# Optimization experiments

Hardware: AMD Instinct MI355X
Metric: run time of the kernel (lower is better)

The kernel has to match this reference:

```python
import jax, jax.numpy as jnp
import numpy as np

N = 50000      # nodes
E = 800000     # directed edges (avg degree 16)
F_IN = 128     # dataset.num_features
H = 256        # hidden_channels
C = 40         # dataset.num_classes


def _glorot(k, shape):
    lim = float(np.sqrt(6.0 / (shape[0] + shape[1])))
    return jax.random.uniform(k, shape, jnp.float32, -lim, lim)


def setup_inputs() -> dict:
    key = jax.random.key(0)
    ks = jax.random.split(key, 8)
    x = jax.random.normal(ks[0], (N, F_IN), jnp.float32)
    edge_index = jax.random.randint(ks[1], (2, E), 0, N, dtype=jnp.int32)
    W1 = _glorot(ks[2], (F_IN, H));      b1 = jnp.zeros((H,), jnp.float32)
    W2 = _glorot(ks[3], (H, H // 2));    b2 = jnp.zeros((H // 2,), jnp.float32)
    W3 = _glorot(ks[4], (H // 2, H // 4)); b3 = jnp.zeros((H // 4,), jnp.float32)
    W4 = _glorot(ks[5], (H // 4, C));    b4 = jnp.zeros((C,), jnp.float32)
    return {"x": x, "edge_index": edge_index,
            "W1": W1, "b1": b1, "W2": W2, "b2": b2,
            "W3": W3, "b3": b3, "W4": W4, "b4": b4}


def reference(x, edge_index, W1, b1, W2, b2, W3, b3, W4, b4):
    # GCNConv with default add_self_loops=True and symmetric normalization.
    loops = jnp.arange(N, dtype=edge_index.dtype)
    src = jnp.concatenate([edge_index[0], loops])   # message sources
    dst = jnp.concatenate([edge_index[1], loops])   # aggregation targets
    # degree computed on target index (PyG default), incl. self-loops
    deg = jax.ops.segment_sum(jnp.ones_like(dst, jnp.float32), dst, num_segments=N)
    dinv = jnp.where(deg > 0, jax.lax.rsqrt(deg), 0.0)
    norm = dinv[src] * dinv[dst]                    # [E+N]

    def conv(h, W, b):
        h = h @ W                                   # transform first (PyG order)
        msg = h[src] * norm[:, None]                # gather + scale
        return jax.ops.segment_sum(msg, dst, num_segments=N) + b

    h = jax.nn.relu(conv(x, W1, b1))   # dropout = identity in eval mode
    h = jax.nn.relu(conv(h, W2, b2))
    h = jax.nn.relu(conv(h, W3, b3))
    return conv(h, W4, b4)
```

## Files before the change

### kernel.cpp

```cpp
#include <hip/hip_runtime.h>
#include <stdint.h>

#define NNODES 50000
#define NEDGES 800000
#define NB ((NNODES + 255) / 256)
#define EPB 4096
#define SCAT_NBLK ((NEDGES + EPB - 1) / EPB)

typedef __attribute__((ext_vector_type(8))) short bf16x8;
typedef __attribute__((ext_vector_type(4))) float f32x4;

__device__ inline unsigned short f2bf(float f) {
    unsigned u = __float_as_uint(f);
    return (unsigned short)((u + 0x7fffu + ((u >> 16) & 1u)) >> 16);
}
__device__ inline float bf2f(unsigned short h) {
    return __uint_as_float(((unsigned)h) << 16);
}


__global__ void zero_kernel(int* __restrict__ p, int n) {
    int i = blockIdx.x * blockDim.x + threadIdx.x;
    if (i < n) p[i] = 0;
}

__global__ __launch_bounds__(256) void bucket_count_kernel(const int* __restrict__ dst,
                                                           int* __restrict__ bhist) {
    __shared__ int h[NB];
    for (int b = threadIdx.x; b < NB; b += 256) h[b] = 0;
    __syncthreads();
    const int base = blockIdx.x * EPB;
#pragma unroll
    for (int i = 0; i < EPB / 256; ++i) {
        const int e = base + threadIdx.x + i * 256;
        if (e < NEDGES) atomicAdd(&h[dst[e] >> 8], 1);
    }
    __syncthreads();
    for (int b = threadIdx.x; b < NB; b += 256)
        if (h[b]) atomicAdd(&bhist[b], h[b]);
}

__global__ __launch_bounds__(256) void bucket_scan_kernel(const int* __restrict__ bhist,
                                                          int* __restrict__ bofs,
                                                          int* __restrict__ gcur,
                                                          int* __restrict__ rp_last) {
    __shared__ int s[256];
    const int t = threadIdx.x;
    s[t] = (t < NB) ? bhist[t] : 0;
    __syncthreads();
    for (int off = 1; off < 256; off <<= 1) {
        int v = (t >= off) ? s[t - off] : 0;
        __syncthreads();
        s[t] += v;
        __syncthreads();
    }
    if (t < NB) {
        const int excl = (t > 0) ? s[t - 1] : 0;
        bofs[t] = excl;
        gcur[t] = excl;
    }
    if (t == 255) { bofs[NB] = s[255]; rp_last[0] = s[255]; }
}

__global__ __launch_bounds__(256) void bucket_scatter_kernel(const int* __restrict__ src,
                                                             const int* __restrict__ dst,
                                                             int* __restrict__ gcur,
                                                             unsigned* __restrict__ gpk) {
    __shared__ int h[256];
    __shared__ int s[256];
    __shared__ int gof[256];
    __shared__ unsigned pr[EPB];
    __shared__ int ga[EPB];

    const int t = threadIdx.x;
    const int base = blockIdx.x * EPB;
    const int nval = min(EPB, NEDGES - base);

    h[t] = 0;
    __syncthreads();
#pragma unroll
    for (int i = 0; i < EPB / 256; ++i) {
        const int e = base + t + i * 256;
        if (e < NEDGES) atomicAdd(&h[dst[e] >> 8], 1);
    }
    __syncthreads();
    s[t] = h[t];
    __syncthreads();
    for (int off = 1; off < 256; off <<= 1) {
        int v = (t >= off) ? s[t - off] : 0;
        __syncthreads();
        s[t] += v;
        __syncthreads();
    }
    {
        const int c = h[t];
        if (t < NB && c > 0) gof[t] = atomicAdd(&gcur[t], c);
        const int lofs = s[t] - c;
        h[t] = lofs;
        s[t] = lofs;
    }
    __syncthreads();
#pragma unroll
    for (int i = 0; i < EPB / 256; ++i) {
        const int e = base + t + i * 256;
        if (e < NEDGES) {
            const int d = dst[e];
            const int b = d >> 8;
            const int slot = atomicAdd(&h[b], 1);
            pr[slot] = ((unsigned)(d & 255) << 16) | (unsigned)src[e];
            ga[slot] = gof[b] + (slot - s[b]);
        }
    }
    __syncthreads();
#pragma unroll
    for (int i = 0; i < EPB / 256; ++i) {
        const int slot = t + i * 256;
        if (slot < nval) gpk[ga[slot]] = pr[slot];
    }
}

__global__ __launch_bounds__(256) void csr_fill_kernel(const unsigned* __restrict__ gpk,
                                                       const int* __restrict__ bofs,
                                                       int* __restrict__ rp,
                                                       float* __restrict__ dinv,
                                                       unsigned short* __restrict__ col) {
    __shared__ int c[256];
    __shared__ int s[256];
    __shared__ int cur[256];
    const int t = threadIdx.x;
    const int b = blockIdx.x;
    const int beg = bofs[b], end = bofs[b + 1];
    c[t] = 0;
    __syncthreads();
    for (int e = beg + t; e < end; e += 256) atomicAdd(&c[gpk[e] >> 16], 1);
    __syncthreads();
    s[t] = c[t];
    __syncthreads();
    for (int off = 1; off < 256; off <<= 1) {
        int v = (t >= off) ? s[t - off] : 0;
        __syncthreads();
        s[t] += v;
        __syncthreads();
    }
    const int excl = s[t] - c[t];
    cur[t] = excl;
    const int node = b * 256 + t;
    if (node < NNODES) {
        rp[node] = beg + excl;
        dinv[node] = rsqrtf((float)(c[t] + 1));
    }
    __syncthreads();
    for (int e = beg + t; e < end; e += 256) {
        const unsigned p = gpk[e];
        const int r = atomicAdd(&cur[p >> 16], 1);
        col[beg + r] = (unsigned short)(p & 0xffffu);
    }
}


__global__ __launch_bounds__(256) void cvt_kernel(const float* __restrict__ in,
                                                  const float* __restrict__ dinv,
                                                  unsigned short* __restrict__ out, int n4) {
    int i = blockIdx.x * 256 + threadIdx.x;
    if (i >= n4) return;
    const float dv = dinv[i >> 5];
    float4 v = *(const float4*)(in + (size_t)i * 4);
    ushort4 h;
    h.x = f2bf(dv * v.x); h.y = f2bf(dv * v.y); h.z = f2bf(dv * v.z); h.w = f2bf(dv * v.w);
    *(ushort4*)(out + (size_t)i * 4) = h;
}


template <bool RELU, bool HAS_BIAS>
__global__ __launch_bounds__(256) void agg128_kernel(const float* __restrict__ in32,
                                                     const unsigned short* __restrict__ inbf,
                                                     float* __restrict__ out,
                                                     const int* __restrict__ rp,
                                                     const unsigned short* __restrict__ col,
                                                     const float* __restrict__ dinv,
                                                     const float* __restrict__ bias) {
    const int wave = threadIdx.x >> 6;
    const int lane = threadIdx.x & 63;
    const int d = blockIdx.x * 4 + wave;
    if (d >= NNODES) return;
    const int quarter = lane >> 4;
    const int fl = lane & 15;
    const float dv = dinv[d];

    float acc[8] = {0.f, 0.f, 0.f, 0.f, 0.f, 0.f, 0.f, 0.f};
    if (quarter == 0) {
        float4 s0 = *(const float4*)(in32 + (size_t)d * 128 + fl * 8);
        float4 s1 = *(const float4*)(in32 + (size_t)d * 128 + fl * 8 + 4);
        acc[0] = dv * s0.x; acc[1] = dv * s0.y; acc[2] = dv * s0.z; acc[3] = dv * s0.w;
        acc[4] = dv * s1.x; acc[5] = dv * s1.y; acc[6] = dv * s1.z; acc[7] = dv * s1.w;
    }

    int j = rp[d] + quarter;
    const int end = rp[d + 1];
    for (; j + 12 < end; j += 16) {
        const int c0 = col[j], c1 = col[j + 4], c2 = col[j + 8], c3 = col[j + 12];
        bf16x8 a0 = *(const bf16x8*)(inbf + (size_t)c0 * 128 + fl * 8);
        bf16x8 a1 = *(const bf16x8*)(inbf + (size_t)c1 * 128 + fl * 8);
        bf16x8 a2 = *(const bf16x8*)(inbf + (size_t)c2 * 128 + fl * 8);
        bf16x8 a3 = *(const bf16x8*)(inbf + (size_t)c3 * 128 + fl * 8);
#pragma unroll
        for (int k = 0; k < 8; ++k)
            acc[k] += (bf2f((unsigned short)a0[k]) + bf2f((unsigned short)a1[k])) +
                      (bf2f((unsigned short)a2[k]) + bf2f((unsigned short)a3[k]));
    }
    for (; j + 4 < end; j += 8) {
        const int c0 = col[j], c1 = col[j + 4];
        bf16x8 a0 = *(const bf16x8*)(inbf + (size_t)c0 * 128 + fl * 8);
        bf16x8 a1 = *(const bf16x8*)(inbf + (size_t)c1 * 128 + fl * 8);
#pragma unroll
        for (int k = 0; k < 8; ++k)
            acc[k] += bf2f((unsigned short)a0[k]) + bf2f((unsigned short)a1[k]);
    }
    if (j < end) {
        const int c0 = col[j];
        bf16x8 a0 = *(const bf16x8*)(inbf + (size_t)c0 * 128 + fl * 8);
#pragma unroll
        for (int k = 0; k < 8; ++k) acc[k] += bf2f((unsigned short)a0[k]);
    }

#pragma unroll
    for (int v = 0; v < 8; ++v) {
        acc[v] += __shfl_down(acc[v], 32);
        acc[v] += __shfl_down(acc[v], 16);
    }

    if (quarter == 0) {
        float r[8];
#pragma unroll
        for (int v = 0; v < 8; ++v) {
            float t = dv * acc[v];
            if constexpr (HAS_BIAS) t += bias[fl * 8 + v];
            if constexpr (RELU) t = fmaxf(t, 0.0f);
            r[v] = t;
        }
        *(float4*)(out + (size_t)d * 128 + fl * 8)     = make_float4(r[0], r[1], r[2], r[3]);
        *(float4*)(out + (size_t)d * 128 + fl * 8 + 4) = make_float4(r[4], r[5], r[6], r[7]);
    }
}

template <bool RELU, bool HAS_BIAS, bool WRITE_BF>
__global__ __launch_bounds__(256) void agg64_kernel(const float* __restrict__ in32,
                                                    const unsigned short* __restrict__ inbf,
                                                    float* __restrict__ out,
                                                    unsigned short* __restrict__ outbf,
                                                    const int* __restrict__ rp,
                                                    const unsigned short* __restrict__ col,
                                                    const float* __restrict__ dinv,
                                                    const float* __restrict__ bias) {
    const int wave = threadIdx.x >> 6;
    const int lane = threadIdx.x & 63;
    const int d = blockIdx.x * 4 + wave;
    if (d >= NNODES) return;
    const int eighth = lane >> 3;
    const int fl = lane & 7;
    const float dv = dinv[d];

    float acc[8] = {0.f, 0.f, 0.f, 0.f, 0.f, 0.f, 0.f, 0.f};
    if (eighth == 0) {
        float4 s0 = *(const float4*)(in32 + (size_t)d * 64 + fl * 8);
        float4 s1 = *(const float4*)(in32 + (size_t)d * 64 + fl * 8 + 4);
        acc[0] = dv * s0.x; acc[1] = dv * s0.y; acc[2] = dv * s0.z; acc[3] = dv * s0.w;
        acc[4] = dv * s1.x; acc[5] = dv * s1.y; acc[6] = dv * s1.z; acc[7] = dv * s1.w;
    }

    int j = rp[d] + eighth;
    const int end = rp[d + 1];
    for (; j + 8 < end; j += 16) {
        const int c0 = col[j], c1 = col[j + 8];
        bf16x8 a0 = *(const bf16x8*)(inbf + (size_t)c0 * 64 + fl * 8);
        bf16x8 a1 = *(const bf16x8*)(inbf + (size_t)c1 * 64 + fl * 8);
#pragma unroll
        for (int k = 0; k < 8; ++k)
            acc[k] += bf2f((unsigned short)a0[k]) + bf2f((unsigned short)a1[k]);
    }
    if (j < end) {
        const int c0 = col[j];
        bf16x8 a0 = *(const bf16x8*)(inbf + (size_t)c0 * 64 + fl * 8);
#pragma unroll
        for (int k = 0; k < 8; ++k) acc[k] += bf2f((unsigned short)a0[k]);
    }

#pragma unroll
    for (int v = 0; v < 8; ++v) {
        acc[v] += __shfl_down(acc[v], 32);
        acc[v] += __shfl_down(acc[v], 16);
        acc[v] += __shfl_down(acc[v], 8);
    }

    if (eighth == 0) {
        float r[8];
#pragma unroll
        for (int v = 0; v < 8; ++v) {
            float t = dv * acc[v];
            if constexpr (HAS_BIAS) t += bias[fl * 8 + v];
            if constexpr (RELU) t = fmaxf(t, 0.0f);
            r[v] = t;
        }
        *(float4*)(out + (size_t)d * 64 + fl * 8)     = make_float4(r[0], r[1], r[2], r[3]);
        *(float4*)(out + (size_t)d * 64 + fl * 8 + 4) = make_float4(r[4], r[5], r[6], r[7]);
        if constexpr (WRITE_BF) {
            ushort4 h0, h1;
            h0.x = f2bf(dv * r[0]); h0.y = f2bf(dv * r[1]);
            h0.z = f2bf(dv * r[2]); h0.w = f2bf(dv * r[3]);
            h1.x = f2bf(dv * r[4]); h1.y = f2bf(dv * r[5]);
            h1.z = f2bf(dv * r[6]); h1.w = f2bf(dv * r[7]);
            *(ushort4*)(outbf + (size_t)d * 64 + fl * 8)     = h0;
            *(ushort4*)(outbf + (size_t)d * 64 + fl * 8 + 4) = h1;
        }
    }
}


template <int K, int M>
__global__ __launch_bounds__(256) void repack_kernel(const float* __restrict__ W,
                                                     unsigned short* __restrict__ hi,
                                                     unsigned short* __restrict__ lo) {
    int i = blockIdx.x * 256 + threadIdx.x;
    if (i >= K * M) return;
    const int k = i / M, n = i % M;
    constexpr int KS = K / 32;
    const int cb = n >> 7;
    const int ct = (n >> 4) & 7;
    const int ln = ((k >> 3) & 3) * 16 + (n & 15);
    const int j  = k & 7;
    const int ks = k >> 5;
    const size_t o = ((((size_t)cb * KS + ks) * 8 + ct) * 64 + ln) * 8 + j;
    const float f = W[i];
    const unsigned short h = f2bf(f);
    hi[o] = h;
    lo[o] = f2bf(f - bf2f(h));
}


template <int K, int M, int BM, bool BIAS_RELU, bool WRITE_BF>
__global__ __launch_bounds__(256) void mfma_gemm_kernel(const float* __restrict__ A,
                                                        const unsigned short* __restrict__ Whi,
                                                        const unsigned short* __restrict__ Wlo,
                                                        const float* __restrict__ bias,
                                                        float* __restrict__ C,
                                                        unsigned short* __restrict__ Cbf,
                                                        const float* __restrict__ dinv) {
    constexpr int KS = K / 32;
    constexpr int ASZ = BM * 64;
    constexpr int CI = (BM == 128) ? 4 : 2;
    __shared__ char lds[2 * ASZ + 16384];
    char* Ahi = lds;
    char* Alo = lds + ASZ;
    char* Bhi = lds + 2 * ASZ;
    char* Blo = lds + 2 * ASZ + 8192;

    const int t = threadIdx.x;
    const int lane = t & 63;
    const int w = t >> 6;
    const int wr = (BM == 128) ? (w >> 1) : 0;
    const int wc = (BM == 128) ? (w & 1) : w;
    const int r0 = blockIdx.x * BM;
    const int n0 = blockIdx.y * 128;

    const unsigned short* bhg = Whi + (size_t)blockIdx.y * KS * 4096;
    const unsigned short* blg = Wlo + (size_t)blockIdx.y * KS * 4096;

    f32x4 acc[4][CI];
#pragma unroll
    for (int i = 0; i < 4; ++i)
#pragma unroll
        for (int j = 0; j < CI; ++j) acc[i][j] = (f32x4){0.f, 0.f, 0.f, 0.f};

    for (int ks = 0; ks < KS; ++ks) {
        const int k0 = ks * 32;

        {
            const char* gh = (const char*)(bhg + (size_t)ks * 4096);
            const char* gl = (const char*)(blg + (size_t)ks * 4096);
#pragma unroll
            for (int c = 0; c < 2; ++c) {
                const int ct = w * 2 + c;
                __builtin_amdgcn_global_load_lds(
                    (const __attribute__((address_space(1))) void*)(gh + ct * 1024 + lane * 16),
                    (__attribute__((address_space(3))) void*)(Bhi + ct * 1024), 16, 0, 0);
                __builtin_amdgcn_global_load_lds(
                    (const __attribute__((address_space(1))) void*)(gl + ct * 1024 + lane * 16),
                    (__attribute__((address_space(3))) void*)(Blo + ct * 1024), 16, 0, 0);
            }
        }

        float4 av[BM / 32];
#pragma unroll
        for (int i = 0; i < BM / 32; ++i) {
            const int q = t + i * 256;
            const int row = q >> 3;
            const int kq = (q & 7) * 4;
            const int gr = r0 + row;
            float4 v = make_float4(0.f, 0.f, 0.f, 0.f);
            if (gr < NNODES) v = *(const float4*)(A + (size_t)gr * K + k0 + kq);
            av[i] = v;
        }
#pragma unroll
        for (int i = 0; i < BM / 32; ++i) {
            const int q = t + i * 256;
            const int row = q >> 3;
            const int kq = (q & 7) * 4;
            const int rt = row >> 4, m = row & 15, quad = kq >> 3, j0 = kq & 7;
            const int off = rt * 1024 + (quad * 16 + m) * 16 + j0 * 2;
            const float4 v = av[i];
            ushort4 h, l;
            h.x = f2bf(v.x); l.x = f2bf(v.x - bf2f(h.x));
            h.y = f2bf(v.y); l.y = f2bf(v.y - bf2f(h.y));
            h.z = f2bf(v.z); l.z = f2bf(v.z - bf2f(h.z));
            h.w = f2bf(v.w); l.w = f2bf(v.w - bf2f(h.w));
            *(ushort4*)(Ahi + off) = h;
            *(ushort4*)(Alo + off) = l;
        }
        __syncthreads();

        bf16x8 ah[4], al[4], bh[CI], bl[CI];
#pragma unroll
        for (int i = 0; i < 4; ++i) {
            ah[i] = *(const bf16x8*)(Ahi + (wr * 4 + i) * 1024 + lane * 16);
            al[i] = *(const bf16x8*)(Alo + (wr * 4 + i) * 1024 + lane * 16);
        }
#pragma unroll
        for (int j = 0; j < CI; ++j) {
            bh[j] = *(const bf16x8*)(Bhi + (wc * CI + j) * 1024 + lane * 16);
            bl[j] = *(const bf16x8*)(Blo + (wc * CI + j) * 1024 + lane * 16);
        }
#pragma unroll
        for (int i = 0; i < 4; ++i)
#pragma unroll
            for (int j = 0; j < CI; ++j) {
                acc[i][j] = __builtin_amdgcn_mfma_f32_16x16x32_bf16(ah[i], bh[j], acc[i][j], 0, 0, 0);
                acc[i][j] = __builtin_amdgcn_mfma_f32_16x16x32_bf16(ah[i], bl[j], acc[i][j], 0, 0, 0);
                acc[i][j] = __builtin_amdgcn_mfma_f32_16x16x32_bf16(al[i], bh[j], acc[i][j], 0, 0, 0);
            }
        __syncthreads();
    }

    const int quad = lane >> 4;
    const int cl = lane & 15;
#pragma unroll
    for (int i = 0; i < 4; ++i) {
#pragma unroll
        for (int j = 0; j < CI; ++j) {
            const int colg = n0 + wc * (CI * 16) + j * 16 + cl;
            float bv = 0.f;
            if constexpr (BIAS_RELU) bv = bias[colg];
#pragma unroll
            for (int r = 0; r < 4; ++r) {
                const int rowg = r0 + wr * 64 + i * 16 + quad * 4 + r;
                if (rowg < NNODES) {
                    float v = acc[i][j][r] + bv;
                    if constexpr (BIAS_RELU) v = fmaxf(v, 0.f);
                    C[(size_t)rowg * M + colg] = v;
                    if constexpr (WRITE_BF) Cbf[(size_t)rowg * M + colg] = f2bf(dinv[rowg] * v);
                }
            }
        }
    }
}


template <int BM, int BN, int BK, int TM, int TN, bool HAS_BIAS, bool RELU, bool WRITE_BF>
__global__ __launch_bounds__(256) void gemm_kernel(const float* __restrict__ A,
                                                   const float* __restrict__ W,
                                                   const float* __restrict__ bias,
                                                   float* __restrict__ C,
                                                   unsigned short* __restrict__ Cbf,
                                                   const float* __restrict__ dinv,
                                                   int Nrows, int K, int M) {
    constexpr int TX = BN / TN;
    constexpr int TY = BM / TM;
    static_assert(TX * TY == 256, "thread grid must be 256");
    constexpr int A_LOADS = (BM * BK) / (256 * 4);
    constexpr int W_LOADS = (BN * BK) / (256 * 4);
    static_assert(A_LOADS >= 1 && W_LOADS >= 1, "tile too small");

    const int tid = threadIdx.x;
    const int tx = tid % TX;
    const int ty = tid / TX;
    const int r0 = blockIdx.x * BM;
    const int c0 = blockIdx.y * BN;

    __shared__ float As[BK][BM + 4];
    __shared__ float Ws[BK][BN];

    float acc[TM][TN] = {};

    for (int k0 = 0; k0 < K; k0 += BK) {
#pragma unroll
        for (int l = 0; l < A_LOADS; ++l) {
            const int idx = tid + l * 256;
            const int row = idx / (BK / 4);
            const int kq = idx % (BK / 4);
            float4 v = make_float4(0.f, 0.f, 0.f, 0.f);
            const int gr = r0 + row;
            if (gr < Nrows) v = *(const float4*)(A + (size_t)gr * K + k0 + kq * 4);
            As[kq * 4 + 0][row] = v.x;
            As[kq * 4 + 1][row] = v.y;
            As[kq * 4 + 2][row] = v.z;
            As[kq * 4 + 3][row] = v.w;
        }
#pragma unroll
        for (int l = 0; l < W_LOADS; ++l) {
            const int idx = tid + l * 256;
            const int kk = idx / (BN / 4);
            const int cq = idx % (BN / 4);
            const int gc = c0 + cq * 4;
            float4 v;
            const float* wrow = W + (size_t)(k0 + kk) * M;
            if (gc + 3 < M) {
                v = *(const float4*)(wrow + gc);
            } else {
                v.x = (gc + 0 < M) ? wrow[gc + 0] : 0.f;
                v.y = (gc + 1 < M) ? wrow[gc + 1] : 0.f;
                v.z = (gc + 2 < M) ? wrow[gc + 2] : 0.f;
                v.w = (gc + 3 < M) ? wrow[gc + 3] : 0.f;
            }
            *(float4*)&Ws[kk][cq * 4] = v;
        }
        __syncthreads();

#pragma unroll
        for (int kk = 0; kk < BK; ++kk) {
            float a[TM], b[TN];
#pragma unroll
            for (int i = 0; i < TM; ++i) a[i] = As[kk][ty * TM + i];
#pragma unroll
            for (int j = 0; j < TN; ++j) b[j] = Ws[kk][tx * TN + j];
#pragma unroll
            for (int i = 0; i < TM; ++i)
#pragma unroll
                for (int j = 0; j < TN; ++j) acc[i][j] += a[i] * b[j];
        }
        __syncthreads();
    }

#pragma unroll
    for (int i = 0; i < TM; ++i) {
        const int gr = r0 + ty * TM + i;
        if (gr >= Nrows) continue;
        const float dvr = WRITE_BF ? dinv[gr] : 0.f;
#pragma unroll
        for (int j = 0; j < TN; ++j) {
            const int gc = c0 + tx * TN + j;
            if (gc >= M) continue;
            float v = acc[i][j];
            if constexpr (HAS_BIAS) v += bias[gc];
            if constexpr (RELU) v = fmaxf(v, 0.0f);
            C[(size_t)gr * M + gc] = v;
            if constexpr (WRITE_BF) Cbf[(size_t)gr * M + gc] = f2bf(dvr * v);
        }
    }
}


extern "C" void kernel_launch(void* const* d_in, const int* in_sizes, int n_in,
                              void* d_out, int out_size, void* d_ws, size_t ws_size,
                              hipStream_t stream) {
    const float* x  = (const float*)d_in[0];
    const int* ei   = (const int*)d_in[1];
    const float* W1 = (const float*)d_in[2];
    const float* b1 = (const float*)d_in[3];
    const float* W2 = (const float*)d_in[4];
    const float* b2 = (const float*)d_in[5];
    const float* W3 = (const float*)d_in[6];
    const float* b3 = (const float*)d_in[7];
    const float* W4 = (const float*)d_in[8];
    const float* b4 = (const float*)d_in[9];
    float* out = (float*)d_out;
    const int* esrc = ei;
    const int* edst = ei + NEDGES;

    char* w = (char*)d_ws;
    auto alloc = [&](size_t bytes) -> void* {
        void* p = (void*)w;
        w += (bytes + 255) & ~(size_t)255;
        return p;
    };
    int* rp     = (int*)alloc((size_t)(NNODES + 1) * 4);
    unsigned short* col = (unsigned short*)alloc((size_t)NEDGES * 2);
    float* dinv = (float*)alloc((size_t)NNODES * 4);
    int* bhist  = (int*)alloc((size_t)NB * 4);
    int* bofs   = (int*)alloc((size_t)(NB + 1) * 4);
    int* gcur   = (int*)alloc((size_t)NB * 4);
    unsigned* gpk = (unsigned*)alloc((size_t)NEDGES * 4);
    unsigned short* W1hi = (unsigned short*)alloc((size_t)128 * 256 * 2);
    unsigned short* W1lo = (unsigned short*)alloc((size_t)128 * 256 * 2);
    unsigned short* W2hi = (unsigned short*)alloc((size_t)256 * 128 * 2);
    unsigned short* W2lo = (unsigned short*)alloc((size_t)256 * 128 * 2);
    float* B0   = (float*)alloc((size_t)NNODES * 256 * 4);
    float* B1   = (float*)alloc((size_t)NNODES * 128 * 4);
    float* B2   = (float*)alloc((size_t)NNODES * 128 * 4);
    unsigned short* xbf  = (unsigned short*)alloc((size_t)NNODES * 128 * 2);
    unsigned short* B1bf = (unsigned short*)alloc((size_t)NNODES * 128 * 2);
    unsigned short* B0bf = (unsigned short*)alloc((size_t)NNODES * 64 * 2);
    unsigned short* B3bf = (unsigned short*)alloc((size_t)NNODES * 64 * 2);

    repack_kernel<128, 256><<<(128 * 256 + 255) / 256, 256, 0, stream>>>(W1, W1hi, W1lo);
    repack_kernel<256, 128><<<(256 * 128 + 255) / 256, 256, 0, stream>>>(W2, W2hi, W2lo);

    zero_kernel<<<1, 256, 0, stream>>>(bhist, NB);
    bucket_count_kernel<<<SCAT_NBLK, 256, 0, stream>>>(edst, bhist);
    bucket_scan_kernel<<<1, 256, 0, stream>>>(bhist, bofs, gcur, rp + NNODES);
    bucket_scatter_kernel<<<SCAT_NBLK, 256, 0, stream>>>(esrc, edst, gcur, gpk);
    csr_fill_kernel<<<NB, 256, 0, stream>>>(gpk, bofs, rp, dinv, col);

    cvt_kernel<<<(NNODES * 128 / 4 + 255) / 256, 256, 0, stream>>>(x, dinv, xbf, NNODES * 128 / 4);

    const int aggGrid = (NNODES + 3) / 4;
    const int rowBlks64 = (NNODES + 63) / 64;

    agg128_kernel<false, false><<<aggGrid, 256, 0, stream>>>(x, xbf, B2, rp, col, dinv, nullptr);
    mfma_gemm_kernel<128, 256, 64, true, false>
        <<<dim3(rowBlks64, 2), 256, 0, stream>>>(B2, W1hi, W1lo, b1, B0, nullptr, nullptr);

    mfma_gemm_kernel<256, 128, 64, false, true>
        <<<dim3(rowBlks64, 1), 256, 0, stream>>>(B0, W2hi, W2lo, nullptr, B1, B1bf, dinv);
    agg128_kernel<true, true><<<aggGrid, 256, 0, stream>>>(B1, B1bf, B2, rp, col, dinv, b2);

    gemm_kernel<64, 64, 16, 4, 4, false, false, true>
        <<<dim3(rowBlks64, 1), 256, 0, stream>>>(B2, W3, nullptr, B0, B0bf, dinv, NNODES, 128, 64);
    agg64_kernel<true, true, true><<<aggGrid, 256, 0, stream>>>(B0, B0bf, B1, B3bf, rp, col, dinv, b3);

    agg64_kernel<false, false, false><<<aggGrid, 256, 0, stream>>>(B1, B3bf, B2, nullptr, rp, col, dinv, nullptr);
    gemm_kernel<64, 64, 16, 4, 4, true, false, false>
        <<<dim3(rowBlks64, 1), 256, 0, stream>>>(B2, W4, b4, out, nullptr, nullptr, NNODES, 64, 40);
}
```

Baseline: 336.4 us.

## Fuse layer-1 and layer-2 GEMMs and fold x conversion into CSR fill

Merges the two split-bf16 MFMA GEMMs (128→256 with bias+ReLU, then 256→128) into one kernel. The 64x256 hidden tile stays in LDS as hi/lo bf16, so the 50000x256 fp32 intermediate is never written to or read back from global memory. Weights are now read directly from global into registers instead of staged through LDS. The separate x→bf16 conversion kernel is folded into csr_fill, which saves one launch. In exchange the fused kernel uses about 72KB of LDS per block, which lowers occupancy, and it launches only one block per 64 rows.

Result: no change. 337.2 us (+0.2%).

```diff
diff --git a/kernel.cpp b/kernel.cpp
--- a/kernel.cpp
+++ b/kernel.cpp
@@ -123,10 +123,13 @@
                                                        const int* __restrict__ bofs,
                                                        int* __restrict__ rp,
                                                        float* __restrict__ dinv,
-                                                       unsigned short* __restrict__ col) {
+                                                       unsigned short* __restrict__ col,
+                                                       const float* __restrict__ x,
+                                                       unsigned short* __restrict__ xbf) {
     __shared__ int c[256];
     __shared__ int s[256];
     __shared__ int cur[256];
+    __shared__ float sdv[256];
     const int t = threadIdx.x;
     const int b = blockIdx.x;
     const int beg = bofs[b], end = bofs[b + 1];
@@ -145,9 +148,11 @@
     const int excl = s[t] - c[t];
     cur[t] = excl;
     const int node = b * 256 + t;
+    const float dv = rsqrtf((float)(c[t] + 1));
+    sdv[t] = dv;
     if (node < NNODES) {
         rp[node] = beg + excl;
-        dinv[node] = rsqrtf((float)(c[t] + 1));
+        dinv[node] = dv;
     }
     __syncthreads();
     for (int e = beg + t; e < end; e += 256) {
@@ -155,19 +160,18 @@
         const int r = atomicAdd(&cur[p >> 16], 1);
         col[beg + r] = (unsigned short)(p & 0xffffu);
     }
-}
-
-
-__global__ __launch_bounds__(256) void cvt_kernel(const float* __restrict__ in,
-                                                  const float* __restrict__ dinv,
-                                                  unsigned short* __restrict__ out, int n4) {
-    int i = blockIdx.x * 256 + threadIdx.x;
-    if (i >= n4) return;
-    const float dv = dinv[i >> 5];
-    float4 v = *(const float4*)(in + (size_t)i * 4);
-    ushort4 h;
-    h.x = f2bf(dv * v.x); h.y = f2bf(dv * v.y); h.z = f2bf(dv * v.z); h.w = f2bf(dv * v.w);
-    *(ushort4*)(out + (size_t)i * 4) = h;
+    const int nrows = min(256, NNODES - b * 256);
+    const float* xb = x + (size_t)b * 256 * 128;
+    unsigned short* ob = xbf + (size_t)b * 256 * 128;
+    const int n4 = nrows * 32;
+    for (int i = t; i < n4; i += 256) {
+        const float dv2 = sdv[i >> 5];
+        float4 v = *(const float4*)(xb + (size_t)i * 4);
+        ushort4 hh;
+        hh.x = f2bf(dv2 * v.x); hh.y = f2bf(dv2 * v.y);
+        hh.z = f2bf(dv2 * v.z); hh.w = f2bf(dv2 * v.w);
+        *(ushort4*)(ob + (size_t)i * 4) = hh;
+    }
 }
 
 
@@ -336,77 +340,54 @@
     lo[o] = f2bf(f - bf2f(h));
 }
 
-
-template <int K, int M, int BM, bool BIAS_RELU, bool WRITE_BF>
-__global__ __launch_bounds__(256) void mfma_gemm_kernel(const float* __restrict__ A,
-                                                        const unsigned short* __restrict__ Whi,
-                                                        const unsigned short* __restrict__ Wlo,
-                                                        const float* __restrict__ bias,
+__global__ __launch_bounds__(256) void fused_l12_kernel(const float* __restrict__ A,
+                                                        const unsigned short* __restrict__ W1hi,
+                                                        const unsigned short* __restrict__ W1lo,
+                                                        const float* __restrict__ b1,
+                                                        const unsigned short* __restrict__ W2hi,
+                                                        const unsigned short* __restrict__ W2lo,
                                                         float* __restrict__ C,
                                                         unsigned short* __restrict__ Cbf,
                                                         const float* __restrict__ dinv) {
-    constexpr int KS = K / 32;
-    constexpr int ASZ = BM * 64;
-    constexpr int CI = (BM == 128) ? 4 : 2;
-    __shared__ char lds[2 * ASZ + 16384];
+    __shared__ char lds[8192 + 65536];
     char* Ahi = lds;
-    char* Alo = lds + ASZ;
-    char* Bhi = lds + 2 * ASZ;
-    char* Blo = lds + 2 * ASZ + 8192;
+    char* Alo = lds + 4096;
+    char* Hhi = lds + 8192;
+    char* Hlo = lds + 8192 + 32768;
 
     const int t = threadIdx.x;
     const int lane = t & 63;
     const int w = t >> 6;
-    const int wr = (BM == 128) ? (w >> 1) : 0;
-    const int wc = (BM == 128) ? (w & 1) : w;
-    const int r0 = blockIdx.x * BM;
-    const int n0 = blockIdx.y * 128;
-
-    const unsigned short* bhg = Whi + (size_t)blockIdx.y * KS * 4096;
-    const unsigned short* blg = Wlo + (size_t)blockIdx.y * KS * 4096;
-
-    f32x4 acc[4][CI];
+    const int r0 = blockIdx.x * 64;
+    const int quad = lane >> 4;
+    const int cl = lane & 15;
+
+    f32x4 acc1[4][4];
 #pragma unroll
     for (int i = 0; i < 4; ++i)
 #pragma unroll
-        for (int j = 0; j < CI; ++j) acc[i][j] = (f32x4){0.f, 0.f, 0.f, 0.f};
-
-    for (int ks = 0; ks < KS; ++ks) {
+        for (int j = 0; j < 4; ++j) acc1[i][j] = (f32x4){0.f, 0.f, 0.f, 0.f};
+
+    for (int ks = 0; ks < 4; ++ks) {
         const int k0 = ks * 32;
-
-        {
-            const char* gh = (const char*)(bhg + (size_t)ks * 4096);
-            const char* gl = (const char*)(blg + (size_t)ks * 4096);
-#pragma unroll
-            for (int c = 0; c < 2; ++c) {
-                const int ct = w * 2 + c;
-                __builtin_amdgcn_global_load_lds(
-                    (const __attribute__((address_space(1))) void*)(gh + ct * 1024 + lane * 16),
-                    (__attribute__((address_space(3))) void*)(Bhi + ct * 1024), 16, 0, 0);
-                __builtin_amdgcn_global_load_lds(
-                    (const __attribute__((address_space(1))) void*)(gl + ct * 1024 + lane * 16),
-                    (__attribute__((address_space(3))) void*)(Blo + ct * 1024), 16, 0, 0);
-            }
-        }
-
-        float4 av[BM / 32];
-#pragma unroll
-        for (int i = 0; i < BM / 32; ++i) {
+        float4 av[2];
+#pragma unroll
+        for (int i = 0; i < 2; ++i) {
             const int q = t + i * 256;
             const int row = q >> 3;
             const int kq = (q & 7) * 4;
             const int gr = r0 + row;
             float4 v = make_float4(0.f, 0.f, 0.f, 0.f);
-            if (gr < NNODES) v = *(const float4*)(A + (size_t)gr * K + k0 + kq);
+            if (gr < NNODES) v = *(const float4*)(A + (size_t)gr * 128 + k0 + kq);
             av[i] = v;
         }
 #pragma unroll
-        for (int i = 0; i < BM / 32; ++i) {
+        for (int i = 0; i < 2; ++i) {
             const int q = t + i * 256;
             const int row = q >> 3;
             const int kq = (q & 7) * 4;
-            const int rt = row >> 4, m = row & 15, quad = kq >> 3, j0 = kq & 7;
-            const int off = rt * 1024 + (quad * 16 + m) * 16 + j0 * 2;
+            const int rt = row >> 4, m = row & 15, qd = kq >> 3, j0 = kq & 7;
+            const int off = rt * 1024 + (qd * 16 + m) * 16 + j0 * 2;
             const float4 v = av[i];
             ushort4 h, l;
             h.x = f2bf(v.x); l.x = f2bf(v.x - bf2f(h.x));
@@ -418,49 +399,94 @@
         }
         __syncthreads();
 
-        bf16x8 ah[4], al[4], bh[CI], bl[CI];
+        bf16x8 ah[4], al[4];
 #pragma unroll
         for (int i = 0; i < 4; ++i) {
-            ah[i] = *(const bf16x8*)(Ahi + (wr * 4 + i) * 1024 + lane * 16);
-            al[i] = *(const bf16x8*)(Alo + (wr * 4 + i) * 1024 + lane * 16);
-        }
-#pragma unroll
-        for (int j = 0; j < CI; ++j) {
-            bh[j] = *(const bf16x8*)(Bhi + (wc * CI + j) * 1024 + lane * 16);
-            bl[j] = *(const bf16x8*)(Blo + (wc * CI + j) * 1024 + lane * 16);
+            ah[i] = *(const bf16x8*)(Ahi + i * 1024 + lane * 16);
+            al[i] = *(const bf16x8*)(Alo + i * 1024 + lane * 16);
+        }
+        const size_t wbase = (size_t)((((w >> 1) * 4 + ks) * 8 + (w & 1) * 4)) * 512;
+        bf16x8 bh[4], bl[4];
+#pragma unroll
+        for (int jj = 0; jj < 4; ++jj) {
+            bh[jj] = *(const bf16x8*)(W1hi + wbase + jj * 512 + lane * 8);
+            bl[jj] = *(const bf16x8*)(W1lo + wbase + jj * 512 + lane * 8);
         }
 #pragma unroll
         for (int i = 0; i < 4; ++i)
 #pragma unroll
-            for (int j = 0; j < CI; ++j) {
-                acc[i][j] = __builtin_amdgcn_mfma_f32_16x16x32_bf16(ah[i], bh[j], acc[i][j], 0, 0, 0);
-                acc[i][j] = __builtin_amdgcn_mfma_f32_16x16x32_bf16(ah[i], bl[j], acc[i][j], 0, 0, 0);
-                acc[i][j] = __builtin_amdgcn_mfma_f32_16x16x32_bf16(al[i], bh[j], acc[i][j], 0, 0, 0);
+            for (int jj = 0; jj < 4; ++jj) {
+                acc1[i][jj] = __builtin_amdgcn_mfma_f32_16x16x32_bf16(ah[i], bh[jj], acc1[i][jj], 0, 0, 0);
+                acc1[i][jj] = __builtin_amdgcn_mfma_f32_16x16x32_bf16(ah[i], bl[jj], acc1[i][jj], 0, 0, 0);
+                acc1[i][jj] = __builtin_amdgcn_mfma_f32_16x16x32_bf16(al[i], bh[jj], acc1[i][jj], 0, 0, 0);
             }
         __syncthreads();
     }
 
-    const int quad = lane >> 4;
-    const int cl = lane & 15;
-#pragma unroll
-    for (int i = 0; i < 4; ++i) {
-#pragma unroll
-        for (int j = 0; j < CI; ++j) {
-            const int colg = n0 + wc * (CI * 16) + j * 16 + cl;
-            float bv = 0.f;
-            if constexpr (BIAS_RELU) bv = bias[colg];
+#pragma unroll
+    for (int i = 0; i < 4; ++i)
+#pragma unroll
+        for (int jj = 0; jj < 4; ++jj) {
+            const int colk = w * 64 + jj * 16 + cl;
+            const float bv = b1[colk];
 #pragma unroll
             for (int r = 0; r < 4; ++r) {
-                const int rowg = r0 + wr * 64 + i * 16 + quad * 4 + r;
+                const float v = fmaxf(acc1[i][jj][r] + bv, 0.f);
+                const int m = quad * 4 + r;
+                const int off = (i * 8 + (colk >> 5)) * 1024 +
+                                (((colk >> 3) & 3) * 16 + m) * 16 + (colk & 7) * 2;
+                const unsigned short h = f2bf(v);
+                *(unsigned short*)(Hhi + off) = h;
+                *(unsigned short*)(Hlo + off) = f2bf(v - bf2f(h));
+            }
+        }
+    __syncthreads();
+
+    f32x4 acc2[4][2];
+#pragma unroll
+    for (int i = 0; i < 4; ++i)
+#pragma unroll
+        for (int j = 0; j < 2; ++j) acc2[i][j] = (f32x4){0.f, 0.f, 0.f, 0.f};
+
+    for (int ks2 = 0; ks2 < 8; ++ks2) {
+        bf16x8 a2h[4], a2l[4];
+#pragma unroll
+        for (int i = 0; i < 4; ++i) {
+            a2h[i] = *(const bf16x8*)(Hhi + (i * 8 + ks2) * 1024 + lane * 16);
+            a2l[i] = *(const bf16x8*)(Hlo + (i * 8 + ks2) * 1024 + lane * 16);
+        }
+        bf16x8 b2h[2], b2l[2];
+#pragma unroll
+        for (int j = 0; j < 2; ++j) {
+            const size_t o = (size_t)((ks2 * 8 + w * 2 + j)) * 512;
+            b2h[j] = *(const bf16x8*)(W2hi + o + lane * 8);
+            b2l[j] = *(const bf16x8*)(W2lo + o + lane * 8);
+        }
+#pragma unroll
+        for (int i = 0; i < 4; ++i)
+#pragma unroll
+            for (int j = 0; j < 2; ++j) {
+                acc2[i][j] = __builtin_amdgcn_mfma_f32_16x16x32_bf16(a2h[i], b2h[j], acc2[i][j], 0, 0, 0);
+                acc2[i][j] = __builtin_amdgcn_mfma_f32_16x16x32_bf16(a2h[i], b2l[j], acc2[i][j], 0, 0, 0);
+                acc2[i][j] = __builtin_amdgcn_mfma_f32_16x16x32_bf16(a2l[i], b2h[j], acc2[i][j], 0, 0, 0);
+            }
+    }
+
+#pragma unroll
+    for (int i = 0; i < 4; ++i)
+#pragma unroll
+        for (int j = 0; j < 2; ++j) {
+            const int colg = w * 32 + j * 16 + cl;
+#pragma unroll
+            for (int r = 0; r < 4; ++r) {
+                const int rowg = r0 + i * 16 + quad * 4 + r;
                 if (rowg < NNODES) {
-                    float v = acc[i][j][r] + bv;
-                    if constexpr (BIAS_RELU) v = fmaxf(v, 0.f);
-                    C[(size_t)rowg * M + colg] = v;
-                    if constexpr (WRITE_BF) Cbf[(size_t)rowg * M + colg] = f2bf(dinv[rowg] * v);
+                    const float v = acc2[i][j][r];
+                    C[(size_t)rowg * 128 + colg] = v;
+                    Cbf[(size_t)rowg * 128 + colg] = f2bf(dinv[rowg] * v);
                 }
             }
         }
-    }
 }
 
 
@@ -607,19 +633,14 @@
     bucket_count_kernel<<<SCAT_NBLK, 256, 0, stream>>>(edst, bhist);
     bucket_scan_kernel<<<1, 256, 0, stream>>>(bhist, bofs, gcur, rp + NNODES);
     bucket_scatter_kernel<<<SCAT_NBLK, 256, 0, stream>>>(esrc, edst, gcur, gpk);
-    csr_fill_kernel<<<NB, 256, 0, stream>>>(gpk, bofs, rp, dinv, col);
-
-    cvt_kernel<<<(NNODES * 128 / 4 + 255) / 256, 256, 0, stream>>>(x, dinv, xbf, NNODES * 128 / 4);
+    csr_fill_kernel<<<NB, 256, 0, stream>>>(gpk, bofs, rp, dinv, col, x, xbf);
 
     const int aggGrid = (NNODES + 3) / 4;
     const int rowBlks64 = (NNODES + 63) / 64;
 
     agg128_kernel<false, false><<<aggGrid, 256, 0, stream>>>(x, xbf, B2, rp, col, dinv, nullptr);
-    mfma_gemm_kernel<128, 256, 64, true, false>
-        <<<dim3(rowBlks64, 2), 256, 0, stream>>>(B2, W1hi, W1lo, b1, B0, nullptr, nullptr);
-
-    mfma_gemm_kernel<256, 128, 64, false, true>
-        <<<dim3(rowBlks64, 1), 256, 0, stream>>>(B0, W2hi, W2lo, nullptr, B1, B1bf, dinv);
+    fused_l12_kernel<<<rowBlks64, 256, 0, stream>>>(B2, W1hi, W1lo, b1, W2hi, W2lo, B1, B1bf, dinv);
+
     agg128_kernel<true, true><<<aggGrid, 256, 0, stream>>>(B1, B1bf, B2, rp, col, dinv, b2);
 
     gemm_kernel<64, 64, 16, 4, 4, false, false, true>
```

## Store GEMM activations as pre-split bf16 hi/lo and fold x conversion into CSR fill

Applied to the files above, without the earlier changes.

The x-to-bf16 conversion is folded into the CSR fill kernel, which removes a separate launch. The first aggregation and the layer-1 GEMM now write their outputs as split bf16 hi/lo pairs in row-major order. The rewritten MFMA GEMM then loads A tiles straight into LDS and reads W fragments from global memory, instead of converting fp32 A inside the GEMM and staging W through LDS. Each block now covers all output columns, so the 2-column-block grid is gone. This saves per-GEMM conversion work and some LDS traffic, but adds extra hi/lo stores, scattered 2-byte epilogue writes, and uncached W reads from global memory.

After: 355.5 us. 1.06x slower.

```diff
diff --git a/kernel.cpp b/kernel.cpp
--- a/kernel.cpp
+++ b/kernel.cpp
@@ -123,10 +123,13 @@
                                                        const int* __restrict__ bofs,
                                                        int* __restrict__ rp,
                                                        float* __restrict__ dinv,
-                                                       unsigned short* __restrict__ col) {
+                                                       unsigned short* __restrict__ col,
+                                                       const float* __restrict__ x,
+                                                       unsigned short* __restrict__ xbf) {
     __shared__ int c[256];
     __shared__ int s[256];
     __shared__ int cur[256];
+    __shared__ float sdv[256];
     const int t = threadIdx.x;
     const int b = blockIdx.x;
     const int beg = bofs[b], end = bofs[b + 1];
@@ -145,9 +148,11 @@
     const int excl = s[t] - c[t];
     cur[t] = excl;
     const int node = b * 256 + t;
+    const float dv = rsqrtf((float)(c[t] + 1));
+    sdv[t] = dv;
     if (node < NNODES) {
         rp[node] = beg + excl;
-        dinv[node] = rsqrtf((float)(c[t] + 1));
+        dinv[node] = dv;
     }
     __syncthreads();
     for (int e = beg + t; e < end; e += 256) {
@@ -155,26 +160,27 @@
         const int r = atomicAdd(&cur[p >> 16], 1);
         col[beg + r] = (unsigned short)(p & 0xffffu);
     }
-}
-
-
-__global__ __launch_bounds__(256) void cvt_kernel(const float* __restrict__ in,
-                                                  const float* __restrict__ dinv,
-                                                  unsigned short* __restrict__ out, int n4) {
-    int i = blockIdx.x * 256 + threadIdx.x;
-    if (i >= n4) return;
-    const float dv = dinv[i >> 5];
-    float4 v = *(const float4*)(in + (size_t)i * 4);
-    ushort4 h;
-    h.x = f2bf(dv * v.x); h.y = f2bf(dv * v.y); h.z = f2bf(dv * v.z); h.w = f2bf(dv * v.w);
-    *(ushort4*)(out + (size_t)i * 4) = h;
-}
-
-
-template <bool RELU, bool HAS_BIAS>
+    const int nrows = min(256, NNODES - b * 256);
+    const float* xb = x + (size_t)b * 256 * 128;
+    unsigned short* ob = xbf + (size_t)b * 256 * 128;
+    const int n4 = nrows * 32;
+    for (int i = t; i < n4; i += 256) {
+        const float dv2 = sdv[i >> 5];
+        float4 v = *(const float4*)(xb + (size_t)i * 4);
+        ushort4 hh;
+        hh.x = f2bf(dv2 * v.x); hh.y = f2bf(dv2 * v.y);
+        hh.z = f2bf(dv2 * v.z); hh.w = f2bf(dv2 * v.w);
+        *(ushort4*)(ob + (size_t)i * 4) = hh;
+    }
+}
+
+
+template <bool RELU, bool HAS_BIAS, bool WRITE_SPLIT>
 __global__ __launch_bounds__(256) void agg128_kernel(const float* __restrict__ in32,
                                                      const unsigned short* __restrict__ inbf,
                                                      float* __restrict__ out,
+                                                     unsigned short* __restrict__ outhi,
+                                                     unsigned short* __restrict__ outlo,
                                                      const int* __restrict__ rp,
                                                      const unsigned short* __restrict__ col,
                                                      const float* __restrict__ dinv,
@@ -238,8 +244,24 @@
             if constexpr (RELU) t = fmaxf(t, 0.0f);
             r[v] = t;
         }
-        *(float4*)(out + (size_t)d * 128 + fl * 8)     = make_float4(r[0], r[1], r[2], r[3]);
-        *(float4*)(out + (size_t)d * 128 + fl * 8 + 4) = make_float4(r[4], r[5], r[6], r[7]);
+        if constexpr (WRITE_SPLIT) {
+            ushort4 h0, h1v, l0, l1v;
+            h0.x = f2bf(r[0]); l0.x = f2bf(r[0] - bf2f(h0.x));
+            h0.y = f2bf(r[1]); l0.y = f2bf(r[1] - bf2f(h0.y));
+            h0.z = f2bf(r[2]); l0.z = f2bf(r[2] - bf2f(h0.z));
+            h0.w = f2bf(r[3]); l0.w = f2bf(r[3] - bf2f(h0.w));
+            h1v.x = f2bf(r[4]); l1v.x = f2bf(r[4] - bf2f(h1v.x));
+            h1v.y = f2bf(r[5]); l1v.y = f2bf(r[5] - bf2f(h1v.y));
+            h1v.z = f2bf(r[6]); l1v.z = f2bf(r[6] - bf2f(h1v.z));
+            h1v.w = f2bf(r[7]); l1v.w = f2bf(r[7] - bf2f(h1v.w));
+            *(ushort4*)(outhi + (size_t)d * 128 + fl * 8)     = h0;
+            *(ushort4*)(outhi + (size_t)d * 128 + fl * 8 + 4) = h1v;
+            *(ushort4*)(outlo + (size_t)d * 128 + fl * 8)     = l0;
+            *(ushort4*)(outlo + (size_t)d * 128 + fl * 8 + 4) = l1v;
+        } else {
+            *(float4*)(out + (size_t)d * 128 + fl * 8)     = make_float4(r[0], r[1], r[2], r[3]);
+            *(float4*)(out + (size_t)d * 128 + fl * 8 + 4) = make_float4(r[4], r[5], r[6], r[7]);
+        }
     }
 }
 
@@ -337,33 +359,31 @@
 }
 
 
-template <int K, int M, int BM, bool BIAS_RELU, bool WRITE_BF>
-__global__ __launch_bounds__(256) void mfma_gemm_kernel(const float* __restrict__ A,
-                                                        const unsigned short* __restrict__ Whi,
-                                                        const unsigned short* __restrict__ Wlo,
-                                                        const float* __restrict__ bias,
-                                                        float* __restrict__ C,
-                                                        unsigned short* __restrict__ Cbf,
-                                                        const float* __restrict__ dinv) {
+template <int K, int M, int EPI>
+__global__ __launch_bounds__(256) void mfma2_kernel(const unsigned short* __restrict__ Ahi_g,
+                                                    const unsigned short* __restrict__ Alo_g,
+                                                    const unsigned short* __restrict__ Whi,
+                                                    const unsigned short* __restrict__ Wlo,
+                                                    const float* __restrict__ bias,
+                                                    float* __restrict__ C,
+                                                    unsigned short* __restrict__ Chi,
+                                                    unsigned short* __restrict__ Clo,
+                                                    unsigned short* __restrict__ Cbf,
+                                                    const float* __restrict__ dinv) {
     constexpr int KS = K / 32;
-    constexpr int ASZ = BM * 64;
-    constexpr int CI = (BM == 128) ? 4 : 2;
-    __shared__ char lds[2 * ASZ + 16384];
+    constexpr int CI = M / 64;
+    __shared__ char lds[8192];
     char* Ahi = lds;
-    char* Alo = lds + ASZ;
-    char* Bhi = lds + 2 * ASZ;
-    char* Blo = lds + 2 * ASZ + 8192;
+    char* Alo = lds + 4096;
 
     const int t = threadIdx.x;
     const int lane = t & 63;
     const int w = t >> 6;
-    const int wr = (BM == 128) ? (w >> 1) : 0;
-    const int wc = (BM == 128) ? (w & 1) : w;
-    const int r0 = blockIdx.x * BM;
-    const int n0 = blockIdx.y * 128;
-
-    const unsigned short* bhg = Whi + (size_t)blockIdx.y * KS * 4096;
-    const unsigned short* blg = Wlo + (size_t)blockIdx.y * KS * 4096;
+    const int r0 = blockIdx.x * 64;
+    const int quad = lane >> 4;
+    const int cl = lane & 15;
+
+    const size_t abase = ((size_t)(r0 + w * 16 + cl) * K + (size_t)quad * 8) * 2;
 
     f32x4 acc[4][CI];
 #pragma unroll
@@ -372,62 +392,29 @@
         for (int j = 0; j < CI; ++j) acc[i][j] = (f32x4){0.f, 0.f, 0.f, 0.f};
 
     for (int ks = 0; ks < KS; ++ks) {
-        const int k0 = ks * 32;
-
-        {
-            const char* gh = (const char*)(bhg + (size_t)ks * 4096);
-            const char* gl = (const char*)(blg + (size_t)ks * 4096);
-#pragma unroll
-            for (int c = 0; c < 2; ++c) {
-                const int ct = w * 2 + c;
-                __builtin_amdgcn_global_load_lds(
-                    (const __attribute__((address_space(1))) void*)(gh + ct * 1024 + lane * 16),
-                    (__attribute__((address_space(3))) void*)(Bhi + ct * 1024), 16, 0, 0);
-                __builtin_amdgcn_global_load_lds(
-                    (const __attribute__((address_space(1))) void*)(gl + ct * 1024 + lane * 16),
-                    (__attribute__((address_space(3))) void*)(Blo + ct * 1024), 16, 0, 0);
-            }
-        }
-
-        float4 av[BM / 32];
-#pragma unroll
-        for (int i = 0; i < BM / 32; ++i) {
-            const int q = t + i * 256;
-            const int row = q >> 3;
-            const int kq = (q & 7) * 4;
-            const int gr = r0 + row;
-            float4 v = make_float4(0.f, 0.f, 0.f, 0.f);
-            if (gr < NNODES) v = *(const float4*)(A + (size_t)gr * K + k0 + kq);
-            av[i] = v;
-        }
-#pragma unroll
-        for (int i = 0; i < BM / 32; ++i) {
-            const int q = t + i * 256;
-            const int row = q >> 3;
-            const int kq = (q & 7) * 4;
-            const int rt = row >> 4, m = row & 15, quad = kq >> 3, j0 = kq & 7;
-            const int off = rt * 1024 + (quad * 16 + m) * 16 + j0 * 2;
-            const float4 v = av[i];
-            ushort4 h, l;
-            h.x = f2bf(v.x); l.x = f2bf(v.x - bf2f(h.x));
-            h.y = f2bf(v.y); l.y = f2bf(v.y - bf2f(h.y));
-            h.z = f2bf(v.z); l.z = f2bf(v.z - bf2f(h.z));
-            h.w = f2bf(v.w); l.w = f2bf(v.w - bf2f(h.w));
-            *(ushort4*)(Ahi + off) = h;
-            *(ushort4*)(Alo + off) = l;
-        }
-        __syncthreads();
-
-        bf16x8 ah[4], al[4], bh[CI], bl[CI];
+        const size_t koff = abase + (size_t)ks * 64;
+        __builtin_amdgcn_global_load_lds(
+            (const __attribute__((address_space(1))) void*)((const char*)Ahi_g + koff),
+            (__attribute__((address_space(3))) void*)(Ahi + w * 1024), 16, 0, 0);
+        __builtin_amdgcn_global_load_lds(
+            (const __attribute__((address_space(1))) void*)((const char*)Alo_g + koff),
+            (__attribute__((address_space(3))) void*)(Alo + w * 1024), 16, 0, 0);
+
+        bf16x8 bh[CI], bl[CI];
+#pragma unroll
+        for (int j = 0; j < CI; ++j) {
+            const int g = w * CI + j;
+            const size_t off = (size_t)(((g >> 3) * KS + ks) * 8 + (g & 7)) * 512 + lane * 8;
+            bh[j] = *(const bf16x8*)(Whi + off);
+            bl[j] = *(const bf16x8*)(Wlo + off);
+        }
+        __syncthreads();
+
+        bf16x8 ah[4], al[4];
 #pragma unroll
         for (int i = 0; i < 4; ++i) {
-            ah[i] = *(const bf16x8*)(Ahi + (wr * 4 + i) * 1024 + lane * 16);
-            al[i] = *(const bf16x8*)(Alo + (wr * 4 + i) * 1024 + lane * 16);
-        }
-#pragma unroll
-        for (int j = 0; j < CI; ++j) {
-            bh[j] = *(const bf16x8*)(Bhi + (wc * CI + j) * 1024 + lane * 16);
-            bl[j] = *(const bf16x8*)(Blo + (wc * CI + j) * 1024 + lane * 16);
+            ah[i] = *(const bf16x8*)(Ahi + i * 1024 + lane * 16);
+            al[i] = *(const bf16x8*)(Alo + i * 1024 + lane * 16);
         }
 #pragma unroll
         for (int i = 0; i < 4; ++i)
@@ -440,27 +427,30 @@
         __syncthreads();
     }
 
-    const int quad = lane >> 4;
-    const int cl = lane & 15;
-#pragma unroll
-    for (int i = 0; i < 4; ++i) {
+#pragma unroll
+    for (int i = 0; i < 4; ++i)
 #pragma unroll
         for (int j = 0; j < CI; ++j) {
-            const int colg = n0 + wc * (CI * 16) + j * 16 + cl;
+            const int colg = (w * CI + j) * 16 + cl;
             float bv = 0.f;
-            if constexpr (BIAS_RELU) bv = bias[colg];
+            if constexpr (EPI == 0) bv = bias[colg];
 #pragma unroll
             for (int r = 0; r < 4; ++r) {
-                const int rowg = r0 + wr * 64 + i * 16 + quad * 4 + r;
+                const int rowg = r0 + i * 16 + quad * 4 + r;
                 if (rowg < NNODES) {
-                    float v = acc[i][j][r] + bv;
-                    if constexpr (BIAS_RELU) v = fmaxf(v, 0.f);
-                    C[(size_t)rowg * M + colg] = v;
-                    if constexpr (WRITE_BF) Cbf[(size_t)rowg * M + colg] = f2bf(dinv[rowg] * v);
+                    if constexpr (EPI == 0) {
+                        const float v = fmaxf(acc[i][j][r] + bv, 0.f);
+                        const unsigned short h = f2bf(v);
+                        Chi[(size_t)rowg * M + colg] = h;
+                        Clo[(size_t)rowg * M + colg] = f2bf(v - bf2f(h));
+                    } else {
+                        const float v = acc[i][j][r];
+                        C[(size_t)rowg * M + colg] = v;
+                        Cbf[(size_t)rowg * M + colg] = f2bf(dinv[rowg] * v);
+                    }
                 }
             }
         }
-    }
 }
 
 
@@ -592,7 +582,11 @@
     unsigned short* W1lo = (unsigned short*)alloc((size_t)128 * 256 * 2);
     unsigned short* W2hi = (unsigned short*)alloc((size_t)256 * 128 * 2);
     unsigned short* W2lo = (unsigned short*)alloc((size_t)256 * 128 * 2);
-    float* B0   = (float*)alloc((size_t)NNODES * 256 * 4);
+    unsigned short* AggHi = (unsigned short*)alloc((size_t)NNODES * 128 * 2);
+    unsigned short* AggLo = (unsigned short*)alloc((size_t)NNODES * 128 * 2);
+    unsigned short* H1hi  = (unsigned short*)alloc((size_t)NNODES * 256 * 2);
+    unsigned short* H1lo  = (unsigned short*)alloc((size_t)NNODES * 256 * 2);
+    float* B0   = (float*)alloc((size_t)NNODES * 64 * 4);
     float* B1   = (float*)alloc((size_t)NNODES * 128 * 4);
     float* B2   = (float*)alloc((size_t)NNODES * 128 * 4);
     unsigned short* xbf  = (unsigned short*)alloc((size_t)NNODES * 128 * 2);
@@ -607,20 +601,19 @@
     bucket_count_kernel<<<SCAT_NBLK, 256, 0, stream>>>(edst, bhist);
     bucket_scan_kernel<<<1, 256, 0, stream>>>(bhist, bofs, gcur, rp + NNODES);
     bucket_scatter_kernel<<<SCAT_NBLK, 256, 0, stream>>>(esrc, edst, gcur, gpk);
-    csr_fill_kernel<<<NB, 256, 0, stream>>>(gpk, bofs, rp, dinv, col);
-
-    cvt_kernel<<<(NNODES * 128 / 4 + 255) / 256, 256, 0, stream>>>(x, dinv, xbf, NNODES * 128 / 4);
+    csr_fill_kernel<<<NB, 256, 0, stream>>>(gpk, bofs, rp, dinv, col, x, xbf);
 
     const int aggGrid = (NNODES + 3) / 4;
     const int rowBlks64 = (NNODES + 63) / 64;
 
-    agg128_kernel<false, false><<<aggGrid, 256, 0, stream>>>(x, xbf, B2, rp, col, dinv, nullptr);
-    mfma_gemm_kernel<128, 256, 64, true, false>
-        <<<dim3(rowBlks64, 2), 256, 0, stream>>>(B2, W1hi, W1lo, b1, B0, nullptr, nullptr);
-
-    mfma_gemm_kernel<256, 128, 64, false, true>
-        <<<dim3(rowBlks64, 1), 256, 0, stream>>>(B0, W2hi, W2lo, nullptr, B1, B1bf, dinv);
-    agg128_kernel<true, true><<<aggGrid, 256, 0, stream>>>(B1, B1bf, B2, rp, col, dinv, b2);
+    agg128_kernel<false, false, true><<<aggGrid, 256, 0, stream>>>(
+        x, xbf, nullptr, AggHi, AggLo, rp, col, dinv, nullptr);
+    mfma2_kernel<128, 256, 0><<<rowBlks64, 256, 0, stream>>>(
+        AggHi, AggLo, W1hi, W1lo, b1, nullptr, H1hi, H1lo, nullptr, nullptr);
+    mfma2_kernel<256, 128, 1><<<rowBlks64, 256, 0, stream>>>(
+        H1hi, H1lo, W2hi, W2lo, nullptr, B1, nullptr, nullptr, B1bf, dinv);
+    agg128_kernel<true, true, false><<<aggGrid, 256, 0, stream>>>(
+        B1, B1bf, B2, nullptr, nullptr, rp, col, dinv, b2);
 
     gemm_kernel<64, 64, 16, 4, 4, false, false, true>
         <<<dim3(rowBlks64, 1), 256, 0, stream>>>(B2, W3, nullptr, B0, B0bf, dinv, NNODES, 128, 64);
```
